# Kernel optimization log

Measured on AMD Instinct MI355X. Metric: run time of the kernel, lower is better.

Reference implementation:

```python
import jax, jax.numpy as jnp
import numpy as np

EPS = 0.001
NUM_HEAD = 4

def _bn(x, g, b, m, v):
    # x: [B,C,H,W]; per-channel affine batchnorm in eval mode
    inv = g / jnp.sqrt(v + EPS)
    return x * inv[None, :, None, None] + (b - m * inv)[None, :, None, None]

def setup_inputs() -> dict:
    key = jax.random.key(0)
    ks = jax.random.split(key, 16)
    B, C, H, W = 8, 256, 40, 40
    C2 = 2 * C
    return {
        "x": jax.random.normal(ks[0], (B, C, H, W), jnp.float32),
        "qkv_w": jax.random.normal(ks[1], (C2, C), jnp.float32) * 0.05,
        "qkv_g": jax.random.uniform(ks[2], (C2,), jnp.float32),
        "qkv_b": jax.random.normal(ks[3], (C2,), jnp.float32) * 0.05,
        "qkv_m": jax.random.normal(ks[4], (C2,), jnp.float32) * 0.05,
        "qkv_v": jax.random.uniform(ks[5], (C2,), jnp.float32) + 0.5,
        "cb1_w": jax.random.normal(ks[6], (C, 1, 3, 3), jnp.float32) * 0.05,
        "cb1_g": jax.random.uniform(ks[7], (C,), jnp.float32),
        "cb1_b": jax.random.normal(ks[8], (C,), jnp.float32) * 0.05,
        "cb1_m": jax.random.normal(ks[9], (C,), jnp.float32) * 0.05,
        "cb1_v": jax.random.uniform(ks[10], (C,), jnp.float32) + 0.5,
        "cb2_w": jax.random.normal(ks[11], (C, C), jnp.float32) * 0.05,
        "cb2_g": jax.random.uniform(ks[12], (C,), jnp.float32),
        "cb2_b": jax.random.normal(ks[13], (C,), jnp.float32) * 0.05,
        "cb2_m": jax.random.normal(ks[14], (C,), jnp.float32) * 0.05,
        "cb2_v": jax.random.uniform(ks[15], (C,), jnp.float32) + 0.5,
    }

def reference(x, qkv_w, qkv_g, qkv_b, qkv_m, qkv_v,
              cb1_w, cb1_g, cb1_b, cb1_m, cb1_v,
              cb2_w, cb2_g, cb2_b, cb2_m, cb2_v):
    B, C, H, W = x.shape
    nh = NUM_HEAD
    dh = C // nh          # dim_head
    dk = dh // 2          # dim_key
    scale = dk ** -0.5
    L = H * W

    # qkv: 1x1 conv (ch -> 2ch) + BN
    qkv = jnp.einsum('oc,bchw->bohw', qkv_w, x)
    qkv = _bn(qkv, qkv_g, qkv_b, qkv_m, qkv_v)
    qkv = qkv.reshape(B, nh, 2 * dk + dh, L)
    q, k, v = qkv[:, :, :dk], qkv[:, :, dk:2 * dk], qkv[:, :, 2 * dk:]

    # attn = q^T @ k * scale -> softmax over last dim
    attn = jnp.einsum('bndq,bndk->bnqk', q, k) * scale  # [B,nh,L,L]
    attn = jax.nn.softmax(attn, axis=-1)

    # y = v @ attn^T : y[d,q] = sum_k v[d,k] * attn[q,k]
    y = jnp.einsum('bndk,bnqk->bndq', v, attn).reshape(B, C, H, W)

    # depthwise 3x3 conv branch on v + BN
    vr = v.reshape(B, C, H, W)
    dw = jax.lax.conv_general_dilated(
        vr, cb1_w, window_strides=(1, 1), padding=((1, 1), (1, 1)),
        feature_group_count=C, dimension_numbers=('NCHW', 'OIHW', 'NCHW'))
    y = y + _bn(dw, cb1_g, cb1_b, cb1_m, cb1_v)

    # final 1x1 conv + BN
    out = jnp.einsum('oc,bchw->bohw', cb2_w, y)
    return _bn(out, cb2_g, cb2_b, cb2_m, cb2_v)
```

## Files before the change

kernel.cpp:

```cpp
#include <hip/hip_runtime.h>
#include <hip/hip_bf16.h>

#define EPS 1e-3f
#define QSC_LOG2E 0.2550348653f

typedef __attribute__((ext_vector_type(8))) short bf16x8;
typedef __attribute__((ext_vector_type(4))) float f32x4;
typedef __attribute__((ext_vector_type(4))) unsigned short u16x4;
typedef __attribute__((ext_vector_type(8))) unsigned short u16x8;
typedef __attribute__((ext_vector_type(2))) unsigned int u32x2;

typedef const __attribute__((address_space(1))) unsigned int g_u32;
typedef __attribute__((address_space(3))) unsigned int l_u32;

__device__ __forceinline__ unsigned short f2bf(float f) {
    union { float f; unsigned u; } v; v.f = f;
    unsigned r = v.u + 0x7FFFu + ((v.u >> 16) & 1u);
    return (unsigned short)(r >> 16);
}
__device__ __forceinline__ float bf2f(unsigned short h) {
    union { unsigned u; float f; } v; v.u = ((unsigned)h) << 16;
    return v.f;
}
__device__ __forceinline__ unsigned pkbf(float lo, float hi) {
    float2 t; t.x = lo; t.y = hi;
    __hip_bfloat162 h = __float22bfloat162_rn(t);
    union { __hip_bfloat162 h; unsigned u; } c; c.h = h;
    return c.u;
}

__global__ __launch_bounds__(256) void conv_kernel(
    const float* __restrict__ wq, const float* __restrict__ wc,
    unsigned short* __restrict__ wqb, unsigned short* __restrict__ wcb,
    const float* __restrict__ x, unsigned short* __restrict__ xt)
{
    int bid = blockIdx.x;
    int tid = threadIdx.x;
    if (bid < 192) {
        int i = (bid * 256 + tid) * 4;
        const float* src; unsigned short* dst; int off;
        if (i < 131072) { src = wq; dst = wqb; off = i; }
        else            { src = wc; dst = wcb; off = i - 131072; }
        f32x4 v = *(const f32x4*)(src + off);
        u16x4 o;
        #pragma unroll
        for (int j = 0; j < 4; ++j) o[j] = f2bf(v[j]);
        *(u16x4*)(dst + off) = o;
        return;
    }
    __shared__ float t[64][65];
    int bid2 = bid - 192;
    int l0 = (bid2 % 25) * 64, c0 = ((bid2 / 25) & 3) * 64, b = bid2 / 100;
    const float* xb = x + ((size_t)b * 256 + c0) * 1600 + l0;
    #pragma unroll
    for (int p = 0; p < 4; ++p) {
        int row = p * 16 + (tid >> 4);
        int col = (tid & 15) * 4;
        f32x4 v = *(const f32x4*)(xb + (size_t)row * 1600 + col);
        #pragma unroll
        for (int j = 0; j < 4; ++j) t[row][col + j] = v[j];
    }
    __syncthreads();
    int l = tid >> 2, cs = tid & 3;
    u16x8 o0, o1;
    #pragma unroll
    for (int i = 0; i < 8; ++i) o0[i] = f2bf(t[cs * 16 + i][l]);
    #pragma unroll
    for (int i = 0; i < 8; ++i) o1[i] = f2bf(t[cs * 16 + 8 + i][l]);
    unsigned short* dst = xt + ((size_t)b * 1600 + l0 + l) * 256 + c0 + cs * 16;
    *(u16x8*)dst = o0;
    *(u16x8*)(dst + 8) = o1;
}

__global__ __launch_bounds__(256) void qkv_gemm_kernel(
    const unsigned short* __restrict__ wqb, const unsigned short* __restrict__ xt,
    const float* __restrict__ gg, const float* __restrict__ bet,
    const float* __restrict__ mm, const float* __restrict__ vv,
    unsigned short* __restrict__ qk, unsigned short* __restrict__ vt,
    unsigned short* __restrict__ v2)
{
    __shared__ unsigned short ldsT[4][32 * 72];

    const int gl_tile = blockIdx.x % 104;
    const int by = blockIdx.x / 104;
    if (gl_tile >= 100) return;

    const int tid = threadIdx.x, wid = tid >> 6, lane = tid & 63;
    const int g = lane >> 4, cc = lane & 15;
    const int gl0 = gl_tile * 128 + (wid & 1) * 64;
    const int o_base = by * 64 + (wid >> 1) * 32;

    const unsigned short* wb0 = wqb + (size_t)(o_base + cc) * 256;
    const unsigned short* wb1 = wqb + (size_t)(o_base + 16 + cc) * 256;
    const unsigned short* xb  = xt + (size_t)(gl0 + cc) * 256;

    const f32x4 fz = {0.f, 0.f, 0.f, 0.f};
    f32x4 acc[2][4] = {{fz, fz, fz, fz}, {fz, fz, fz, fz}};
    #pragma unroll 4
    for (int kk = 0; kk < 256; kk += 32) {
        bf16x8 a0 = *(const bf16x8*)(wb0 + kk + 8 * g);
        bf16x8 a1 = *(const bf16x8*)(wb1 + kk + 8 * g);
        #pragma unroll
        for (int f = 0; f < 4; ++f) {
            bf16x8 bfr = *(const bf16x8*)(xb + (size_t)f * 16 * 256 + kk + 8 * g);
            acc[0][f] = __builtin_amdgcn_mfma_f32_16x16x32_bf16(a0, bfr, acc[0][f], 0, 0, 0);
            acc[1][f] = __builtin_amdgcn_mfma_f32_16x16x32_bf16(a1, bfr, acc[1][f], 0, 0, 0);
        }
    }

    const int head = by >> 1;
    const bool is_v = by & 1;
    float inv[2][4], bias[2][4];
    #pragma unroll
    for (int i = 0; i < 2; ++i) {
        #pragma unroll
        for (int r = 0; r < 4; ++r) {
            int oc = o_base + 16 * i + 4 * g + r;
            float iv = gg[oc] * rsqrtf(vv[oc] + EPS);
            float bs = bet[oc] - mm[oc] * iv;
            if ((oc & 127) < 32) { iv *= QSC_LOG2E; bs *= QSC_LOG2E; }
            inv[i][r] = iv; bias[i][r] = bs;
        }
    }

    if (!is_v) {
        #pragma unroll
        for (int f = 0; f < 4; ++f) {
            int gl = gl0 + 16 * f + cc;
            int b  = gl / 1600;
            int ll = gl - b * 1600;
            unsigned short* dst = qk + ((size_t)(b * 4 + head) * 1600 + ll) * 64;
            #pragma unroll
            for (int i = 0; i < 2; ++i) {
                u16x4 pk;
                #pragma unroll
                for (int r = 0; r < 4; ++r) pk[r] = f2bf(acc[i][f][r] * inv[i][r] + bias[i][r]);
                *(u16x4*)(dst + (o_base & 63) + 16 * i + 4 * g) = pk;
            }
        }
    } else {
        const int d_base = (o_base & 63);
        #pragma unroll
        for (int f = 0; f < 4; ++f) {
            int gl = gl0 + 16 * f + cc;
            unsigned short* v2dst = v2 + (size_t)gl * 256 + head * 64 + d_base;
            #pragma unroll
            for (int i = 0; i < 2; ++i) {
                u16x4 pk;
                #pragma unroll
                for (int r = 0; r < 4; ++r) {
                    unsigned short h = f2bf(acc[i][f][r] * inv[i][r] + bias[i][r]);
                    pk[r] = h;
                    ldsT[wid][(16 * i + 4 * g + r) * 72 + 16 * f + cc] = h;
                }
                *(u16x4*)(v2dst + 16 * i + 4 * g) = pk;
            }
        }
        asm volatile("s_waitcnt lgkmcnt(0)" ::: "memory");
        #pragma unroll
        for (int j = 0; j < 4; ++j) {
            int p = j * 64 + lane;
            int d_loc = p >> 3, c8 = p & 7;
            u16x8 val = *(const u16x8*)&ldsT[wid][d_loc * 72 + c8 * 8];
            int gl_c = gl0 + c8 * 8;
            int b  = gl_c / 1600;
            int ll = gl_c - b * 1600;
            *(u16x8*)(vt + ((size_t)(b * 4 + head) * 64 + d_base + d_loc) * 1600 + ll) = val;
        }
    }
}

__global__ __launch_bounds__(256) void attn_kernel(
    const unsigned short* __restrict__ qk, const unsigned short* __restrict__ vt,
    unsigned short* __restrict__ pa, unsigned short* __restrict__ pb,
    float* __restrict__ ssum)
{
    __shared__ __align__(16) unsigned short kbuf[2][64 * 32];
    __shared__ __align__(16) unsigned short vbuf[2][64 * 64];

    const int tid = threadIdx.x, wid = tid >> 6, lane = tid & 63;
    const int g = lane >> 4, cc = lane & 15;
    const int combo = blockIdx.x & 63;
    const int pair = combo >> 1;
    const int z = combo & 1;
    const int q0 = (blockIdx.x >> 6) * 64 + wid * 16;

    const int kt_begin = z ? 13 : 0;
    const int NT = z ? 12 : 13;

    const unsigned short* qkb = qk + (size_t)pair * 1600 * 64;
    const unsigned short* vtb = vt + (size_t)pair * 64 * 1600;

    bf16x8 bq = *(const bf16x8*)(qkb + (size_t)(q0 + cc) * 64 + 8 * g);

    const int krow = tid >> 2, kchk = tid & 3;
    const unsigned short* kP = qkb + (size_t)krow * 64 + 32 + (kchk ^ (krow & 3)) * 8
                              + (size_t)kt_begin * 4096;
    const int vrow = tid >> 3, vchk = tid & 7;
    const unsigned short* vPa = vtb + (size_t)vrow * 1600 + (vchk ^ (vrow & 7)) * 8
                              + (size_t)kt_begin * 64;
    const unsigned short* vPb = vPa + (size_t)32 * 1600;

    const unsigned short* kr0  = &kbuf[0][cc * 32 + (g ^ (cc & 3)) * 8];
    const unsigned short* kr1  = &kbuf[1][cc * 32 + (g ^ (cc & 3)) * 8];
    const unsigned short* vr0a = &vbuf[0][cc * 64 + ((g) ^ (cc & 7)) * 8];
    const unsigned short* vr0b = &vbuf[0][cc * 64 + ((4 + g) ^ (cc & 7)) * 8];
    const unsigned short* vr1a = &vbuf[1][cc * 64 + ((g) ^ (cc & 7)) * 8];
    const unsigned short* vr1b = &vbuf[1][cc * 64 + ((4 + g) ^ (cc & 7)) * 8];

    #define STAGE(bufi)                                                               \
        do {                                                                          \
            __builtin_amdgcn_global_load_lds((g_u32*)kP,                              \
                (l_u32*)(&kbuf[bufi][wid * 512]), 16, 0, 0);                          \
            __builtin_amdgcn_global_load_lds((g_u32*)vPa,                             \
                (l_u32*)(&vbuf[bufi][wid * 512]), 16, 0, 0);                          \
            __builtin_amdgcn_global_load_lds((g_u32*)vPb,                             \
                (l_u32*)(&vbuf[bufi][2048 + wid * 512]), 16, 0, 0);                   \
            kP += 4096; vPa += 64; vPb += 64;                                         \
        } while (0)

    const f32x4 fz = {0.f, 0.f, 0.f, 0.f};
    const short one_bf = (short)0x3F80;
    const bf16x8 ones = {one_bf, one_bf, one_bf, one_bf, one_bf, one_bf, one_bf, one_bf};
    f32x4 o[4] = {fz, fz, fz, fz};
    f32x4 sumacc = fz;

    auto compute = [&](const unsigned short* kr, const unsigned short* vra,
                       const unsigned short* vrb) {
        bf16x8 kf[4], vf[8];
        #pragma unroll
        for (int f = 0; f < 4; ++f)
            kf[f] = *(const bf16x8*)(kr + f * 512);
        #pragma unroll
        for (int f2 = 0; f2 < 4; ++f2) {
            vf[2 * f2]     = *(const bf16x8*)(vra + f2 * 1024);
            vf[2 * f2 + 1] = *(const bf16x8*)(vrb + f2 * 1024);
        }

        f32x4 s4[4];
        __builtin_amdgcn_s_setprio(1);
        #pragma unroll
        for (int f = 0; f < 4; ++f)
            s4[f] = __builtin_amdgcn_mfma_f32_16x16x32_bf16(kf[f], bq, fz, 0, 0, 0);
        __builtin_amdgcn_s_setprio(0);

        unsigned c2[4][2];
        #pragma unroll
        for (int f = 0; f < 4; ++f) {
            float p0 = exp2f(s4[f][0]), p1 = exp2f(s4[f][1]);
            float p2 = exp2f(s4[f][2]), p3 = exp2f(s4[f][3]);
            c2[f][0] = pkbf(p0, p1);
            c2[f][1] = pkbf(p2, p3);
        }
        unsigned pb_u[2][4];
        #pragma unroll
        for (int s2 = 0; s2 < 2; ++s2) {
            const int fA = 2 * s2, fB = 2 * s2 + 1;
            u32x2 xy0 = __builtin_amdgcn_permlane32_swap(c2[fA][0], c2[fB][0], false, false);
            u32x2 xy1 = __builtin_amdgcn_permlane32_swap(c2[fA][1], c2[fB][1], false, false);
            u32x2 w02 = __builtin_amdgcn_permlane16_swap(xy0.x, xy0.y, false, false);
            u32x2 w13 = __builtin_amdgcn_permlane16_swap(xy1.x, xy1.y, false, false);
            pb_u[s2][0] = w02.x;
            pb_u[s2][1] = w13.x;
            pb_u[s2][2] = w02.y;
            pb_u[s2][3] = w13.y;
        }

        __builtin_amdgcn_s_setprio(1);
        #pragma unroll
        for (int s2 = 0; s2 < 2; ++s2) {
            union { unsigned u[4]; bf16x8 v; } pbv;
            #pragma unroll
            for (int j = 0; j < 4; ++j) pbv.u[j] = pb_u[s2][j];
            #pragma unroll
            for (int f2 = 0; f2 < 4; ++f2)
                o[f2] = __builtin_amdgcn_mfma_f32_16x16x32_bf16(vf[f2 * 2 + s2], pbv.v, o[f2], 0, 0, 0);
            sumacc = __builtin_amdgcn_mfma_f32_16x16x32_bf16(ones, pbv.v, sumacc, 0, 0, 0);
        }
        __builtin_amdgcn_s_setprio(0);
    };

    STAGE(0);

    for (int t = 0; t + 1 < NT; ++t) {
        STAGE((t + 1) & 1);
        asm volatile("s_waitcnt vmcnt(3)" ::: "memory");
        __builtin_amdgcn_s_barrier();
        if (t & 1) compute(kr1, vr1a, vr1b);
        else       compute(kr0, vr0a, vr0b);
        __builtin_amdgcn_s_barrier();
    }
    asm volatile("s_waitcnt vmcnt(0)" ::: "memory");
    __builtin_amdgcn_s_barrier();
    if ((NT - 1) & 1) compute(kr1, vr1a, vr1b);
    else              compute(kr0, vr0a, vr0b);
    #undef STAGE

    const int n = pair & 3, b = pair >> 2;
    unsigned short* pdst = (z ? pb : pa) + ((size_t)b * 1600 + q0 + cc) * 256 + n * 64;
    #pragma unroll
    for (int f2 = 0; f2 < 4; ++f2) {
        u16x4 st;
        #pragma unroll
        for (int r = 0; r < 4; ++r) st[r] = f2bf(o[f2][r]);
        *(u16x4*)(pdst + 16 * f2 + 4 * g) = st;
    }
    if (lane < 16)
        ssum[((size_t)z * 32 + b * 4 + n) * 1600 + q0 + cc] = sumacc[0];
}

__global__ __launch_bounds__(256) void dwout_kernel(
    const unsigned short* __restrict__ v2,
    const unsigned short* __restrict__ pa, const unsigned short* __restrict__ pb,
    const float* __restrict__ ssum,
    const float* __restrict__ cw, const float* __restrict__ g1,
    const float* __restrict__ b1, const float* __restrict__ m1,
    const float* __restrict__ v1,
    const unsigned short* __restrict__ wcb, const float* __restrict__ g2,
    const float* __restrict__ b2, const float* __restrict__ m2,
    const float* __restrict__ vbn2,
    float* __restrict__ out)
{
    __shared__ unsigned short y2s[32][264];

    const int tid = threadIdx.x, wid = tid >> 6, lane = tid & 63;
    const int g = lane >> 4, cc = lane & 15;
    const int gl0 = blockIdx.x * 32;

    {
        const int gl_loc = tid & 31, cpart = tid >> 5;
        const int gl = gl0 + gl_loc;
        const int b = gl / 1600, l = gl - b * 1600;
        const int h = l / 40, w = l - h * 40;
        #pragma unroll
        for (int cg = 0; cg < 4; ++cg) {
            const int c0 = cpart * 32 + cg * 8;
            const int n = c0 >> 6;
            float s0 = ssum[(size_t)(b * 4 + n) * 1600 + l];
            float s1 = ssum[(size_t)(32 + b * 4 + n) * 1600 + l];
            float il = 1.f / (s0 + s1);
            float s[8];
            #pragma unroll
            for (int i = 0; i < 8; ++i) s[i] = 0.f;
            #pragma unroll
            for (int kh = -1; kh <= 1; ++kh) {
                int hh = h + kh;
                if (hh < 0 || hh >= 40) continue;
                #pragma unroll
                for (int kw = -1; kw <= 1; ++kw) {
                    int ww = w + kw;
                    if (ww < 0 || ww >= 40) continue;
                    u16x8 vv8 = *(const u16x8*)(v2 + (size_t)(gl + kh * 40 + kw) * 256 + c0);
                    const int tap = (kh + 1) * 3 + (kw + 1);
                    #pragma unroll
                    for (int i = 0; i < 8; ++i)
                        s[i] = fmaf(bf2f(vv8[i]), cw[(c0 + i) * 9 + tap], s[i]);
                }
            }
            u16x8 ya = *(const u16x8*)(pa + (size_t)gl * 256 + c0);
            u16x8 yb = *(const u16x8*)(pb + (size_t)gl * 256 + c0);
            u16x8 o8;
            #pragma unroll
            for (int i = 0; i < 8; ++i) {
                int c = c0 + i;
                float iv = g1[c] * rsqrtf(v1[c] + EPS);
                float yv = (bf2f(ya[i]) + bf2f(yb[i])) * il;
                o8[i] = f2bf(yv + s[i] * iv + (b1[c] - m1[c] * iv));
            }
            *(u16x8*)&y2s[gl_loc][c0] = o8;
        }
    }
    __syncthreads();

    const int o_base = wid * 64;
    const unsigned short* wb = wcb + (size_t)(o_base + cc) * 256;

    const f32x4 fz = {0.f, 0.f, 0.f, 0.f};
    f32x4 acc[4][2] = {{fz, fz}, {fz, fz}, {fz, fz}, {fz, fz}};
    #pragma unroll 4
    for (int kk = 0; kk < 256; kk += 32) {
        bf16x8 a[4], bfr[2];
        #pragma unroll
        for (int i = 0; i < 4; ++i)
            a[i] = *(const bf16x8*)(wb + (size_t)i * 16 * 256 + kk + 8 * g);
        #pragma unroll
        for (int f = 0; f < 2; ++f)
            bfr[f] = *(const bf16x8*)&y2s[16 * f + cc][kk + 8 * g];
        #pragma unroll
        for (int i = 0; i < 4; ++i)
            #pragma unroll
            for (int f = 0; f < 2; ++f)
                acc[i][f] = __builtin_amdgcn_mfma_f32_16x16x32_bf16(a[i], bfr[f], acc[i][f], 0, 0, 0);
    }
    #pragma unroll
    for (int i = 0; i < 4; ++i) {
        #pragma unroll
        for (int r = 0; r < 4; ++r) {
            int oc = o_base + 16 * i + 4 * g + r;
            float iv = g2[oc] * rsqrtf(vbn2[oc] + EPS);
            float bs = b2[oc] - m2[oc] * iv;
            #pragma unroll
            for (int f = 0; f < 2; ++f) {
                int gl = gl0 + 16 * f + cc;
                int b  = gl / 1600;
                int ll = gl - b * 1600;
                out[((size_t)b * 256 + oc) * 1600 + ll] = acc[i][f][r] * iv + bs;
            }
        }
    }
}

extern "C" void kernel_launch(void* const* d_in, const int* in_sizes, int n_in,
                              void* d_out, int out_size, void* d_ws, size_t ws_size,
                              hipStream_t stream) {
    const float* x     = (const float*)d_in[0];
    const float* qkv_w = (const float*)d_in[1];
    const float* qkv_g = (const float*)d_in[2];
    const float* qkv_b = (const float*)d_in[3];
    const float* qkv_m = (const float*)d_in[4];
    const float* qkv_v = (const float*)d_in[5];
    const float* cb1_w = (const float*)d_in[6];
    const float* cb1_g = (const float*)d_in[7];
    const float* cb1_b = (const float*)d_in[8];
    const float* cb1_m = (const float*)d_in[9];
    const float* cb1_v = (const float*)d_in[10];
    const float* cb2_w = (const float*)d_in[11];
    const float* cb2_g = (const float*)d_in[12];
    const float* cb2_b = (const float*)d_in[13];
    const float* cb2_m = (const float*)d_in[14];
    const float* cb2_v = (const float*)d_in[15];
    float* out = (float*)d_out;

    unsigned short* ws16 = (unsigned short*)d_ws;
    const size_t N16 = 3276800;
    unsigned short* xt  = ws16;
    unsigned short* qk  = ws16 + N16;
    unsigned short* vt  = ws16 + 2 * N16;
    unsigned short* pb_ = ws16 + 3 * N16;
    unsigned short* v2  = ws16 + 4 * N16;
    unsigned short* wqb = ws16 + 5 * N16;
    unsigned short* wcb = wqb + 131072;
    float* ssum = (float*)(wcb + 65536);
    unsigned short* pa = xt;

    conv_kernel<<<dim3(992), 256, 0, stream>>>(qkv_w, cb2_w, wqb, wcb, x, xt);
    qkv_gemm_kernel<<<dim3(832), 256, 0, stream>>>(wqb, xt, qkv_g, qkv_b, qkv_m, qkv_v, qk, vt, v2);
    attn_kernel<<<dim3(1600), 256, 0, stream>>>(qk, vt, pa, pb_, ssum);
    dwout_kernel<<<dim3(400), 256, 0, stream>>>(v2, pa, pb_, ssum,
                                                cb1_w, cb1_g, cb1_b, cb1_m, cb1_v,
                                                wcb, cb2_g, cb2_b, cb2_m, cb2_v, out);
}
```

Measured before the change: 113.4 us.

## Process two 16-query tiles per wave in attention with 128-thread blocks

The attention kernel now runs 2 waves per block instead of 4, and each wave handles 32 queries as two 16-row MFMA tiles. Each K and V fragment read from LDS is reused for both query tiles, which halves LDS reads per unit of work. Each thread issues twice as many async global-to-LDS loads per stage, with the wait count adjusted to match. The cost is more accumulator registers per wave and fewer waves per block to hide latency.

```diff
diff --git a/kernel.cpp b/kernel.cpp
--- a/kernel.cpp
+++ b/kernel.cpp
@@ -170,7 +170,7 @@
     }
 }
 
-__global__ __launch_bounds__(256) void attn_kernel(
+__global__ __launch_bounds__(128) void attn_kernel(
     const unsigned short* __restrict__ qk, const unsigned short* __restrict__ vt,
     unsigned short* __restrict__ pa, unsigned short* __restrict__ pb,
     float* __restrict__ ssum)
@@ -183,7 +183,7 @@
     const int combo = blockIdx.x & 63;
     const int pair = combo >> 1;
     const int z = combo & 1;
-    const int q0 = (blockIdx.x >> 6) * 64 + wid * 16;
+    const int q0 = (blockIdx.x >> 6) * 64 + wid * 32;
 
     const int kt_begin = z ? 13 : 0;
     const int NT = z ? 12 : 13;
@@ -191,15 +191,15 @@
     const unsigned short* qkb = qk + (size_t)pair * 1600 * 64;
     const unsigned short* vtb = vt + (size_t)pair * 64 * 1600;
 
-    bf16x8 bq = *(const bf16x8*)(qkb + (size_t)(q0 + cc) * 64 + 8 * g);
+    bf16x8 bq0 = *(const bf16x8*)(qkb + (size_t)(q0 + cc) * 64 + 8 * g);
+    bf16x8 bq1 = *(const bf16x8*)(qkb + (size_t)(q0 + 16 + cc) * 64 + 8 * g);
 
     const int krow = tid >> 2, kchk = tid & 3;
     const unsigned short* kP = qkb + (size_t)krow * 64 + 32 + (kchk ^ (krow & 3)) * 8
                               + (size_t)kt_begin * 4096;
     const int vrow = tid >> 3, vchk = tid & 7;
-    const unsigned short* vPa = vtb + (size_t)vrow * 1600 + (vchk ^ (vrow & 7)) * 8
+    const unsigned short* vP = vtb + (size_t)vrow * 1600 + (vchk ^ (vrow & 7)) * 8
                               + (size_t)kt_begin * 64;
-    const unsigned short* vPb = vPa + (size_t)32 * 1600;
 
     const unsigned short* kr0  = &kbuf[0][cc * 32 + (g ^ (cc & 3)) * 8];
     const unsigned short* kr1  = &kbuf[1][cc * 32 + (g ^ (cc & 3)) * 8];
@@ -212,70 +212,86 @@
         do {                                                                          \
             __builtin_amdgcn_global_load_lds((g_u32*)kP,                              \
                 (l_u32*)(&kbuf[bufi][wid * 512]), 16, 0, 0);                          \
-            __builtin_amdgcn_global_load_lds((g_u32*)vPa,                             \
+            __builtin_amdgcn_global_load_lds((g_u32*)(kP + 2048),                     \
+                (l_u32*)(&kbuf[bufi][1024 + wid * 512]), 16, 0, 0);                   \
+            __builtin_amdgcn_global_load_lds((g_u32*)vP,                              \
                 (l_u32*)(&vbuf[bufi][wid * 512]), 16, 0, 0);                          \
-            __builtin_amdgcn_global_load_lds((g_u32*)vPb,                             \
+            __builtin_amdgcn_global_load_lds((g_u32*)(vP + 16 * 1600),                \
+                (l_u32*)(&vbuf[bufi][1024 + wid * 512]), 16, 0, 0);                   \
+            __builtin_amdgcn_global_load_lds((g_u32*)(vP + 32 * 1600),                \
                 (l_u32*)(&vbuf[bufi][2048 + wid * 512]), 16, 0, 0);                   \
-            kP += 4096; vPa += 64; vPb += 64;                                         \
+            __builtin_amdgcn_global_load_lds((g_u32*)(vP + 48 * 1600),                \
+                (l_u32*)(&vbuf[bufi][3072 + wid * 512]), 16, 0, 0);                   \
+            kP += 4096; vP += 64;                                                     \
         } while (0)
 
     const f32x4 fz = {0.f, 0.f, 0.f, 0.f};
     const short one_bf = (short)0x3F80;
     const bf16x8 ones = {one_bf, one_bf, one_bf, one_bf, one_bf, one_bf, one_bf, one_bf};
-    f32x4 o[4] = {fz, fz, fz, fz};
-    f32x4 sumacc = fz;
+    f32x4 o[2][4] = {{fz, fz, fz, fz}, {fz, fz, fz, fz}};
+    f32x4 sumacc[2] = {fz, fz};
 
     auto compute = [&](const unsigned short* kr, const unsigned short* vra,
                        const unsigned short* vrb) {
-        bf16x8 kf[4], vf[8];
-        #pragma unroll
-        for (int f = 0; f < 4; ++f)
-            kf[f] = *(const bf16x8*)(kr + f * 512);
-        #pragma unroll
-        for (int f2 = 0; f2 < 4; ++f2) {
-            vf[2 * f2]     = *(const bf16x8*)(vra + f2 * 1024);
-            vf[2 * f2 + 1] = *(const bf16x8*)(vrb + f2 * 1024);
-        }
-
-        f32x4 s4[4];
+        f32x4 s4[2][4];
+        {
+            bf16x8 kf[4];
+            #pragma unroll
+            for (int f = 0; f < 4; ++f)
+                kf[f] = *(const bf16x8*)(kr + f * 512);
+            __builtin_amdgcn_s_setprio(1);
+            #pragma unroll
+            for (int f = 0; f < 4; ++f)
+                s4[0][f] = __builtin_amdgcn_mfma_f32_16x16x32_bf16(kf[f], bq0, fz, 0, 0, 0);
+            #pragma unroll
+            for (int f = 0; f < 4; ++f)
+                s4[1][f] = __builtin_amdgcn_mfma_f32_16x16x32_bf16(kf[f], bq1, fz, 0, 0, 0);
+            __builtin_amdgcn_s_setprio(0);
+        }
+
+        unsigned pb_u[2][2][4];
+        #pragma unroll
+        for (int qf = 0; qf < 2; ++qf) {
+            unsigned c2[4][2];
+            #pragma unroll
+            for (int f = 0; f < 4; ++f) {
+                float p0 = exp2f(s4[qf][f][0]), p1 = exp2f(s4[qf][f][1]);
+                float p2 = exp2f(s4[qf][f][2]), p3 = exp2f(s4[qf][f][3]);
+                c2[f][0] = pkbf(p0, p1);
+                c2[f][1] = pkbf(p2, p3);
+            }
+            #pragma unroll
+            for (int s2 = 0; s2 < 2; ++s2) {
+                const int fA = 2 * s2, fB = 2 * s2 + 1;
+                u32x2 xy0 = __builtin_amdgcn_permlane32_swap(c2[fA][0], c2[fB][0], false, false);
+                u32x2 xy1 = __builtin_amdgcn_permlane32_swap(c2[fA][1], c2[fB][1], false, false);
+                u32x2 w02 = __builtin_amdgcn_permlane16_swap(xy0.x, xy0.y, false, false);
+                u32x2 w13 = __builtin_amdgcn_permlane16_swap(xy1.x, xy1.y, false, false);
+                pb_u[qf][s2][0] = w02.x;
+                pb_u[qf][s2][1] = w13.x;
+                pb_u[qf][s2][2] = w02.y;
+                pb_u[qf][s2][3] = w13.y;
+            }
+        }
+
         __builtin_amdgcn_s_setprio(1);
         #pragma unroll
-        for (int f = 0; f < 4; ++f)
-            s4[f] = __builtin_amdgcn_mfma_f32_16x16x32_bf16(kf[f], bq, fz, 0, 0, 0);
-        __builtin_amdgcn_s_setprio(0);
-
-        unsigned c2[4][2];
-        #pragma unroll
-        for (int f = 0; f < 4; ++f) {
-            float p0 = exp2f(s4[f][0]), p1 = exp2f(s4[f][1]);
-            float p2 = exp2f(s4[f][2]), p3 = exp2f(s4[f][3]);
-            c2[f][0] = pkbf(p0, p1);
-            c2[f][1] = pkbf(p2, p3);
-        }
-        unsigned pb_u[2][4];
-        #pragma unroll
         for (int s2 = 0; s2 < 2; ++s2) {
-            const int fA = 2 * s2, fB = 2 * s2 + 1;
-            u32x2 xy0 = __builtin_amdgcn_permlane32_swap(c2[fA][0], c2[fB][0], false, false);
-            u32x2 xy1 = __builtin_amdgcn_permlane32_swap(c2[fA][1], c2[fB][1], false, false);
-            u32x2 w02 = __builtin_amdgcn_permlane16_swap(xy0.x, xy0.y, false, false);
-            u32x2 w13 = __builtin_amdgcn_permlane16_swap(xy1.x, xy1.y, false, false);
-            pb_u[s2][0] = w02.x;
-            pb_u[s2][1] = w13.x;
-            pb_u[s2][2] = w02.y;
-            pb_u[s2][3] = w13.y;
-        }
-
-        __builtin_amdgcn_s_setprio(1);
-        #pragma unroll
-        for (int s2 = 0; s2 < 2; ++s2) {
-            union { unsigned u[4]; bf16x8 v; } pbv;
-            #pragma unroll
-            for (int j = 0; j < 4; ++j) pbv.u[j] = pb_u[s2][j];
+            const unsigned short* vr = s2 ? vrb : vra;
+            bf16x8 vf[4];
             #pragma unroll
             for (int f2 = 0; f2 < 4; ++f2)
-                o[f2] = __builtin_amdgcn_mfma_f32_16x16x32_bf16(vf[f2 * 2 + s2], pbv.v, o[f2], 0, 0, 0);
-            sumacc = __builtin_amdgcn_mfma_f32_16x16x32_bf16(ones, pbv.v, sumacc, 0, 0, 0);
+                vf[f2] = *(const bf16x8*)(vr + f2 * 1024);
+            #pragma unroll
+            for (int qf = 0; qf < 2; ++qf) {
+                union { unsigned u[4]; bf16x8 v; } pbv;
+                #pragma unroll
+                for (int j = 0; j < 4; ++j) pbv.u[j] = pb_u[qf][s2][j];
+                #pragma unroll
+                for (int f2 = 0; f2 < 4; ++f2)
+                    o[qf][f2] = __builtin_amdgcn_mfma_f32_16x16x32_bf16(vf[f2], pbv.v, o[qf][f2], 0, 0, 0);
+                sumacc[qf] = __builtin_amdgcn_mfma_f32_16x16x32_bf16(ones, pbv.v, sumacc[qf], 0, 0, 0);
+            }
         }
         __builtin_amdgcn_s_setprio(0);
     };
@@ -284,7 +300,7 @@
 
     for (int t = 0; t + 1 < NT; ++t) {
         STAGE((t + 1) & 1);
-        asm volatile("s_waitcnt vmcnt(3)" ::: "memory");
+        asm volatile("s_waitcnt vmcnt(6)" ::: "memory");
         __builtin_amdgcn_s_barrier();
         if (t & 1) compute(kr1, vr1a, vr1b);
         else       compute(kr0, vr0a, vr0b);
@@ -297,16 +313,21 @@
     #undef STAGE
 
     const int n = pair & 3, b = pair >> 2;
-    unsigned short* pdst = (z ? pb : pa) + ((size_t)b * 1600 + q0 + cc) * 256 + n * 64;
-    #pragma unroll
-    for (int f2 = 0; f2 < 4; ++f2) {
-        u16x4 st;
-        #pragma unroll
-        for (int r = 0; r < 4; ++r) st[r] = f2bf(o[f2][r]);
-        *(u16x4*)(pdst + 16 * f2 + 4 * g) = st;
-    }
-    if (lane < 16)
-        ssum[((size_t)z * 32 + b * 4 + n) * 1600 + q0 + cc] = sumacc[0];
+    #pragma unroll
+    for (int qf = 0; qf < 2; ++qf) {
+        unsigned short* pdst = (z ? pb : pa) + ((size_t)b * 1600 + q0 + qf * 16 + cc) * 256 + n * 64;
+        #pragma unroll
+        for (int f2 = 0; f2 < 4; ++f2) {
+            u16x4 st;
+            #pragma unroll
+            for (int r = 0; r < 4; ++r) st[r] = f2bf(o[qf][f2][r]);
+            *(u16x4*)(pdst + 16 * f2 + 4 * g) = st;
+        }
+    }
+    if (lane < 16) {
+        ssum[((size_t)z * 32 + b * 4 + n) * 1600 + q0 + cc]      = sumacc[0][0];
+        ssum[((size_t)z * 32 + b * 4 + n) * 1600 + q0 + 16 + cc] = sumacc[1][0];
+    }
 }
 
 __global__ __launch_bounds__(256) void dwout_kernel(
@@ -445,7 +466,7 @@
 
     conv_kernel<<<dim3(992), 256, 0, stream>>>(qkv_w, cb2_w, wqb, wcb, x, xt);
     qkv_gemm_kernel<<<dim3(832), 256, 0, stream>>>(wqb, xt, qkv_g, qkv_b, qkv_m, qkv_v, qk, vt, v2);
-    attn_kernel<<<dim3(1600), 256, 0, stream>>>(qk, vt, pa, pb_, ssum);
+    attn_kernel<<<dim3(1600), 128, 0, stream>>>(qk, vt, pa, pb_, ssum);
     dwout_kernel<<<dim3(400), 256, 0, stream>>>(v2, pa, pb_, ssum,
                                                 cb1_w, cb1_g, cb1_b, cb1_m, cb1_v,
                                                 wcb, cb2_g, cb2_b, cb2_m, cb2_v, out);
```

New measurement: 119.5 us. 5.4% more time.
